# Kernel optimization log

Measured on AMD Instinct MI355X. Metric: run time of the kernel, lower is better.

Reference implementation:

```python
import jax, jax.numpy as jnp
import numpy as np

NEG = jnp.float32(-1e30)  # finite stand-in for -inf (keeps grads NaN-free)

B, S = 8, 256


def _inside_logZ(scores, mask):
    """CYK inside algorithm. scores/mask: [B, S, S]. Returns scalar logZ.

    Recurrence (widths w = 1..S-1, processed as a scan over anti-diagonals):
      s[i, i+1] = scores[i, i+1]
      s[i, i+w] = scores[i, i+w] + logsumexp_{k=i+1..i+w-1} (s[i, k] + s[k, i+w])
    logZ = sum_b s[b, 0, lens[b]].
    """
    Bsz, Sl, _ = scores.shape
    lens = mask[:, 0].sum(-1)                    # [B] sentence lengths
    idx = jnp.arange(Sl)
    rows = idx[:, None]                          # [S,1] span start i
    m = idx[None, :]                             # [1,S] split offset (k = i+m)
    km = jnp.clip(rows + m, 0, Sl - 1)           # [S,S] split index k, clipped reads

    def step(s, w):
        # s: [B,S,S] chart. Process all spans of width w at once.
        j = jnp.clip(rows + w, 0, Sl - 1)        # [S,1] span end (clipped)
        left = s[:, rows, km]                    # s[b, i, i+m]      -> [B,S,S]
        right = s[:, km, j]                      # s[b, i+m, i+w]    -> [B,S,S]
        valid = (m >= 1) & (m <= w - 1) & (rows + w < Sl)
        lse = jax.nn.logsumexp(jnp.where(valid, left + right, NEG), axis=-1)  # [B,S]
        diag = scores[:, idx, jnp.clip(idx + w, 0, Sl - 1)]                    # [B,S]
        val = diag + jnp.where(w == 1, 0.0, lse)
        # scatter onto the w-th diagonal; out-of-range (i+w >= S) lanes dropped
        s = s.at[:, idx, idx + w].set(val, mode='drop')
        return s, None

    s0 = jnp.full((Bsz, Sl, Sl), NEG, scores.dtype)
    s, _ = jax.lax.scan(step, s0, jnp.arange(1, Sl))
    return s[jnp.arange(Bsz), 0, lens].sum()


def setup_inputs() -> dict:
    key = jax.random.key(0)
    scores = jax.random.normal(key, (B, S, S), dtype=jnp.float32)
    # strict upper-triangular mask (all sentences full length S-1 tokens)
    mask = jnp.triu(jnp.ones((S, S), dtype=bool), k=1)
    mask = jnp.broadcast_to(mask, (B, S, S))
    return {"scores": scores, "mask": mask}


def reference(scores, mask):
    # forward(scores, mask, target=None, mbr=True): marginals = d logZ / d scores
    marginals = jax.grad(lambda sc: _inside_logZ(sc, mask))(scores)
    return marginals
```

## Files before the change

kernel.cpp:

```cpp
#include <hip/hip_runtime.h>

#define SL 256
#define BATCH 8
#define NT 1024
#define W0 16
#define LDSF 33152
#define TABN 264
#define LDSB ((LDSF + 32 + TABN + 3 * 256) * 4)

__device__ __forceinline__ int rowOff(int j) {
  int jp = (j > 128) ? (256 - j) : j;
  int base = (jp - 1) * 260;
  if (j > 128) base += (jp + 3) & ~3;
  return base;
}

template <int G>
__device__ __forceinline__ float grpSum(float v) {
#pragma unroll
  for (int o = G >> 1; o; o >>= 1) v += __shfl_xor(v, o, 64);
  return v;
}

__device__ __forceinline__ void barrier_lgkm() {
  __builtin_amdgcn_sched_barrier(0);
  asm volatile("s_waitcnt lgkmcnt(0)" ::: "memory");
  __builtin_amdgcn_s_barrier();
  __builtin_amdgcn_sched_barrier(0);
}

__device__ void rescaleE(int tid, float dc, int wcur, float* sh,
                         float* Es1, float* Es2, float* Es3,
                         const int* __restrict__ tab) {
  const int lane = tid & 63, wave = tid >> 6;
  for (int j = 1 + wave; j < SL; j += 16) {
    int jlo = j - wcur; if (jlo < 0) jlo = 0;
    int base = tab[j];
    for (int i = jlo + lane; i < j; i += 64)
      sh[base + i] *= __expf(-dc * (float)(j - i));
  }
  const float f1 = __expf(-dc);
  const float f2 = f1 * f1;
  const float f3 = f2 * f1;
  for (int x = tid; x < SL; x += NT) {
    Es1[x] *= f1; Es2[x] *= f2; Es3[x] *= f3;
  }
}

template <int G>
__device__ void insideP(int wlo, int whi, int t0, int tid,
                        const float* __restrict__ sc, float* __restrict__ sh,
                        float* __restrict__ red, const int* __restrict__ tab,
                        float* __restrict__ Es1, float* __restrict__ Es2,
                        float* __restrict__ Es3) {
  constexpr int LG = (G == 4) ? 2 : (G == 8) ? 3 : (G == 16) ? 4 : 5;
  constexpr int NG = 64 / G;
  const int lane = tid & 63, wv = tid >> 6;
  const int l = lane >> LG, lig = lane & (G - 1);
  const int i = wv * (NG - 1) + l;
  for (int w = wlo; w <= whi; w += 2) {
    const int t = t0 + ((w - wlo) >> 1);
    const float fl = red[16 + ((t - 1) & 1)];
    const unsigned wm1 = (unsigned)(w - 1);
    const unsigned wm2 = (unsigned)(w - 2);
    const bool vw = i < SL - w;
    const bool vw1 = (l < NG - 1) && (i < SL - w - 1);
    const int jw = (i + w < SL) ? i + w : SL - 1;
    const int jw1 = (i + w + 1 < SL) ? i + w + 1 : SL - 1;
    const int ojw = tab[jw], ojw1 = tab[jw1];
    const float scw = sc[i * SL + jw];
    const float scw1 = sc[i * SL + jw1];
    float a0 = 0.f, a1 = 0.f, b0 = 0.f, b1 = 0.f;
    if (vw) {
      for (int s4 = ((i + 1) & ~3) + 4 * lig; s4 < i + w; s4 += 4 * G) {
        float4 rw = *(const float4*)(sh + ojw + s4);
        float4 rw1 = *(const float4*)(sh + ojw1 + s4);
        int4 tv = *(const int4*)(tab + s4);
        float e0 = sh[tv.x + i], e1 = sh[tv.y + i];
        float e2 = sh[tv.z + i], e3 = sh[tv.w + i];
        const int d0 = s4 - i;
        float f0 = ((unsigned)(d0 - 1) < wm1) ? e0 : 0.f;
        float f1 = ((unsigned)(d0    ) < wm1) ? e1 : 0.f;
        float f2 = ((unsigned)(d0 + 1) < wm1) ? e2 : 0.f;
        float f3 = ((unsigned)(d0 + 2) < wm1) ? e3 : 0.f;
        a0 = fmaf(f0, rw.x, a0); a1 = fmaf(f1, rw.y, a1);
        a0 = fmaf(f2, rw.z, a0); a1 = fmaf(f3, rw.w, a1);
        float g0 = ((unsigned)(d0 - 2) < wm2) ? e0 : 0.f;
        float g1 = ((unsigned)(d0 - 1) < wm2) ? e1 : 0.f;
        float g2 = ((unsigned)(d0    ) < wm2) ? e2 : 0.f;
        float g3 = ((unsigned)(d0 + 1) < wm2) ? e3 : 0.f;
        b0 = fmaf(g0, rw1.x, b0); b1 = fmaf(g1, rw1.y, b1);
        b0 = fmaf(g2, rw1.z, b0); b1 = fmaf(g3, rw1.w, b1);
      }
    }
    float accw = grpSum<G>(a0 + a1);
    float accw1 = grpSum<G>(b0 + b1);
    float Ew = __expf(scw) * accw;
    if (vw && lig == 0) {
      sh[ojw + i] = Ew;
      if (accw > 3.5e19f || accw < 3e-16f) red[16 + (t & 1)] = fmaxf(accw, 1e-30f);
    }
    float EwN = __shfl_down(Ew, G, 64);
    if (vw1) {
      float tot = accw1 + Es1[i] * EwN + Ew * Es1[jw];
      if (lig == 0) {
        sh[ojw1 + i] = __expf(scw1) * tot;
        if (tot > 3.5e19f || tot < 3e-16f) red[16 + (t & 1)] = fmaxf(tot, 1e-30f);
      }
    }
    __syncthreads();
    if (fl != 0.f) {
      float dc = (__logf(fl) + 8.0f) / (float)(w - 2);
      rescaleE(tid, dc, w + 1, sh, Es1, Es2, Es3, tab);
      __syncthreads();
      if (tid == 0) { red[16] = 0.f; red[17] = 0.f; }
      __syncthreads();
    }
  }
}

template <int G>
__device__ void insideQ(int wlo, int whi, int t0, int tid,
                        const float* __restrict__ sc, float* __restrict__ sh,
                        float* __restrict__ red, const int* __restrict__ tab,
                        float* __restrict__ Es1, float* __restrict__ Es2,
                        float* __restrict__ Es3) {
  constexpr int LG = (G == 4) ? 2 : 3;
  constexpr int NG = 64 / G;
  constexpr int STR = 4 * G;
  const int lane = tid & 63, wv = tid >> 6;
  const int l = lane >> LG, lig = lane & (G - 1);
  const int i = wv * (NG - 3) + l;
  for (int w = wlo; w <= whi; w += 4) {
    const int t = t0 + ((w - wlo) >> 2);
    const float fl = red[16 + ((t - 1) & 1)];
    const bool v0 = i < SL - w;
    const bool v1 = i < SL - w - 1;
    const bool v2 = i < SL - w - 2;
    const bool v3 = i < SL - w - 3;
    const int j0 = (i + w < SL) ? i + w : SL - 1;
    const int j1 = (i + w + 1 < SL) ? i + w + 1 : SL - 1;
    const int j2 = (i + w + 2 < SL) ? i + w + 2 : SL - 1;
    const int j3 = (i + w + 3 < SL) ? i + w + 3 : SL - 1;
    const int o0 = tab[j0], o1 = tab[j1], o2 = tab[j2], o3 = tab[j3];
    const int rb = i * SL;
    const float s0 = sc[rb + j0], s1 = sc[rb + j1];
    const float s2 = sc[rb + j2], s3 = sc[rb + j3];
    float a0=0.f,a1=0.f,b0=0.f,b1=0.f,c0=0.f,c1=0.f,e4a=0.f,e4b=0.f;
    if (v0) {
      const int kend = i + w;
      const unsigned mA = (unsigned)(w - 1);
      const unsigned mB = (unsigned)(w - 2);
      const unsigned mC = (unsigned)(w - 3);
      const unsigned mD = (unsigned)(w - 4);
      auto mchunk = [&](int s4) {
        float4 r0 = *(const float4*)(sh + o0 + s4);
        float4 r1 = *(const float4*)(sh + o1 + s4);
        float4 r2 = *(const float4*)(sh + o2 + s4);
        float4 r3 = *(const float4*)(sh + o3 + s4);
        int4 tv = *(const int4*)(tab + s4);
        float e0 = sh[tv.x + i], e1 = sh[tv.y + i];
        float e2 = sh[tv.z + i], e3 = sh[tv.w + i];
        const int dd = s4 - i;
        float f0 = ((unsigned)(dd - 1) < mA) ? e0 : 0.f;
        float f1 = ((unsigned)(dd    ) < mA) ? e1 : 0.f;
        float f2 = ((unsigned)(dd + 1) < mA) ? e2 : 0.f;
        float f3 = ((unsigned)(dd + 2) < mA) ? e3 : 0.f;
        a0 = fmaf(f0, r0.x, a0); a1 = fmaf(f1, r0.y, a1);
        a0 = fmaf(f2, r0.z, a0); a1 = fmaf(f3, r0.w, a1);
        float g0 = ((unsigned)(dd - 2) < mB) ? e0 : 0.f;
        float g1 = ((unsigned)(dd - 1) < mB) ? e1 : 0.f;
        float g2 = ((unsigned)(dd    ) < mB) ? e2 : 0.f;
        float g3 = ((unsigned)(dd + 1) < mB) ? e3 : 0.f;
        b0 = fmaf(g0, r1.x, b0); b1 = fmaf(g1, r1.y, b1);
        b0 = fmaf(g2, r1.z, b0); b1 = fmaf(g3, r1.w, b1);
        float h0 = ((unsigned)(dd - 3) < mC) ? e0 : 0.f;
        float h1 = ((unsigned)(dd - 2) < mC) ? e1 : 0.f;
        float h2 = ((unsigned)(dd - 1) < mC) ? e2 : 0.f;
        float h3 = ((unsigned)(dd    ) < mC) ? e3 : 0.f;
        c0 = fmaf(h0, r2.x, c0); c1 = fmaf(h1, r2.y, c1);
        c0 = fmaf(h2, r2.z, c0); c1 = fmaf(h3, r2.w, c1);
        float k0 = ((unsigned)(dd - 4) < mD) ? e0 : 0.f;
        float k1 = ((unsigned)(dd - 3) < mD) ? e1 : 0.f;
        float k2 = ((unsigned)(dd - 2) < mD) ? e2 : 0.f;
        float k3 = ((unsigned)(dd - 1) < mD) ? e3 : 0.f;
        e4a = fmaf(k0, r3.x, e4a); e4b = fmaf(k1, r3.y, e4b);
        e4a = fmaf(k2, r3.z, e4a); e4b = fmaf(k3, r3.w, e4b);
      };
      int s4 = ((i + 1) & ~3) + 4 * lig;
      if (s4 < kend) { mchunk(s4); s4 += STR; }
      for (; s4 + 4 <= kend; s4 += STR) {
        float4 r0 = *(const float4*)(sh + o0 + s4);
        float4 r1 = *(const float4*)(sh + o1 + s4);
        float4 r2 = *(const float4*)(sh + o2 + s4);
        float4 r3 = *(const float4*)(sh + o3 + s4);
        int4 tv = *(const int4*)(tab + s4);
        float e0 = sh[tv.x + i], e1 = sh[tv.y + i];
        float e2 = sh[tv.z + i], e3 = sh[tv.w + i];
        a0 = fmaf(e0, r0.x, a0); a1 = fmaf(e1, r0.y, a1);
        a0 = fmaf(e2, r0.z, a0); a1 = fmaf(e3, r0.w, a1);
        b0 = fmaf(e0, r1.x, b0); b1 = fmaf(e1, r1.y, b1);
        b0 = fmaf(e2, r1.z, b0); b1 = fmaf(e3, r1.w, b1);
        c0 = fmaf(e0, r2.x, c0); c1 = fmaf(e1, r2.y, c1);
        c0 = fmaf(e2, r2.z, c0); c1 = fmaf(e3, r2.w, c1);
        e4a = fmaf(e0, r3.x, e4a); e4b = fmaf(e1, r3.y, e4b);
        e4a = fmaf(e2, r3.z, e4a); e4b = fmaf(e3, r3.w, e4b);
      }
      for (; s4 < kend; s4 += STR) mchunk(s4);
    }
    float A0 = grpSum<G>(a0 + a1);
    float A1 = grpSum<G>(b0 + b1);
    float A2 = grpSum<G>(c0 + c1);
    float A3 = grpSum<G>(e4a + e4b);
    const float es1i = Es1[i], es2i = Es2[i], es3i = Es3[i];
    const float E0 = __expf(s0) * A0;
    const float n10 = __shfl_down(E0, G, 64);
    const float n20 = __shfl_down(E0, 2 * G, 64);
    const float n30 = __shfl_down(E0, 3 * G, 64);
    const float T1 = A1 + es1i * n10 + E0 * Es1[j0];
    const float E1v = __expf(s1) * T1;
    const float n11 = __shfl_down(E1v, G, 64);
    const float n21 = __shfl_down(E1v, 2 * G, 64);
    const float T2 = A2 + es1i * n11 + E1v * Es1[j1] + es2i * n20 + E0 * Es2[j0];
    const float E2v = __expf(s2) * T2;
    const float n12 = __shfl_down(E2v, G, 64);
    const float T3 = A3 + es1i * n12 + E2v * Es1[j2] + es2i * n21 + E1v * Es2[j1]
                        + es3i * n30 + E0 * Es3[j0];
    const float E3v = __expf(s3) * T3;
    if (lig == 0) {
      if (v0)                sh[o0 + i] = E0;
      if (v1 && l <= NG - 2) sh[o1 + i] = E1v;
      if (v2 && l <= NG - 3) sh[o2 + i] = E2v;
      if (v3 && l <= NG - 4) sh[o3 + i] = E3v;
      if (v0 && (A0 > 3.5e19f || A0 < 3e-16f)) red[16 + (t & 1)] = fmaxf(A0, 1e-30f);
      if (v3 && l <= NG - 4 && (T3 > 3.5e19f || T3 < 3e-16f))
        red[16 + (t & 1)] = fmaxf(T3, 1e-30f);
    }
    __syncthreads();
    if (fl != 0.f) {
      float dc = (__logf(fl) + 8.0f) / (float)(w - 3);
      rescaleE(tid, dc, w + 3, sh, Es1, Es2, Es3, tab);
      __syncthreads();
      if (tid == 0) { red[16] = 0.f; red[17] = 0.f; }
      __syncthreads();
    }
  }
}

template <int G>
__device__ void outsideP(int wAhi, int wAlo, int tid, const float* __restrict__ sc,
                         float* __restrict__ gOut, const float* __restrict__ Eg,
                         const float* __restrict__ ETg, float* __restrict__ shH,
                         const int* __restrict__ tab, const float* __restrict__ Es1) {
  constexpr int LG = (G == 4) ? 2 : (G == 8) ? 3 : (G == 16) ? 4 : 5;
  constexpr int NG = 64 / G;
  const int lane = tid & 63, wv = tid >> 6;
  const int l = lane >> LG, lig = lane & (G - 1);
  const int p = wv * (NG - 1) + l;
  for (int wA = wAhi; wA >= wAlo; wA -= 2) {
    const int wB = wA - 1;
    const bool vA = p < SL - wA;
    const bool vB = (l >= 1 || wv == 0) && (p < SL - wB);
    const int qA = p + wA, qB = p + wB;
    const int qAc = (qA < SL) ? qA : SL - 1;
    const int qBc = (qB < SL) ? qB : SL - 1;
    const int oA = tab[qAc], oB = tab[qBc];
    const float scA = sc[p * SL + qAc];
    const float scB = sc[p * SL + qBc];
    float EpA = 0.f, EpB = 0.f;
    if (lig == 0) {
      if (vA) EpA = Eg[p * SL + qA];
      if (vB) EpB = Eg[p * SL + qB];
    }
    float a0 = 0.f, a1 = 0.f, b0 = 0.f, b1 = 0.f;
    if (vA || vB) {
      const float* erA = Eg + (size_t)qAc * SL;
      const float* erB = Eg + (size_t)qBc * SL;
      for (int s4 = ((qA + 1) & ~3) + 4 * lig; s4 < SL; s4 += 4 * G) {
        float4 eA = *(const float4*)(erA + s4);
        float4 eB = *(const float4*)(erB + s4);
        int4 tv = *(const int4*)(tab + s4);
        float h0 = shH[tv.x + p], h1 = shH[tv.y + p];
        float h2 = shH[tv.z + p], h3 = shH[tv.w + p];
        float m0 = (s4 + 0 > qA) ? h0 : 0.f, m1 = (s4 + 1 > qA) ? h1 : 0.f;
        float m2 = (s4 + 2 > qA) ? h2 : 0.f, m3 = (s4 + 3 > qA) ? h3 : 0.f;
        a0 = fmaf(eA.x, m0, a0); a1 = fmaf(eA.y, m1, a1);
        a0 = fmaf(eA.z, m2, a0); a1 = fmaf(eA.w, m3, a1);
        b0 = fmaf(eB.x, m0, b0); b1 = fmaf(eB.y, m1, b1);
        b0 = fmaf(eB.z, m2, b0); b1 = fmaf(eB.w, m3, b1);
      }
      for (int s4 = 4 * lig; s4 < p; s4 += 4 * G) {
        float4 ev = *(const float4*)(ETg + (size_t)p * SL + s4);
        float4 hA = *(const float4*)(shH + oA + s4);
        float4 hB = *(const float4*)(shH + oB + s4);
        a0 = fmaf(ev.x, hA.x, a0); a1 = fmaf(ev.y, hA.y, a1);
        a0 = fmaf(ev.z, hA.z, a0); a1 = fmaf(ev.w, hA.w, a1);
        float n0 = (s4 + 0 < p - 1) ? hB.x : 0.f;
        float n1 = (s4 + 1 < p - 1) ? hB.y : 0.f;
        float n2 = (s4 + 2 < p - 1) ? hB.z : 0.f;
        float n3 = (s4 + 3 < p - 1) ? hB.w : 0.f;
        b0 = fmaf(ev.x, n0, b0); b1 = fmaf(ev.y, n1, b1);
        b0 = fmaf(ev.z, n2, b0); b1 = fmaf(ev.w, n3, b1);
      }
    }
    float accA = grpSum<G>(a0 + a1);
    float accBb = grpSum<G>(b0 + b1);
    float HA = __expf(scA) * accA;
    if (vA && lig == 0) {
      shH[oA + p] = HA;
      gOut[p * SL + qA] = EpA * accA;
    }
    float HAup = __shfl_up(HA, G, 64);
    if (vB) {
      float accB = accBb + (vA ? Es1[qBc] * HA : 0.f)
                         + ((p > 0) ? Es1[p - 1] * HAup : 0.f);
      if (lig == 0) {
        shH[oB + p] = __expf(scB) * accB;
        gOut[p * SL + qB] = EpB * accB;
      }
    }
    barrier_lgkm();
  }
}

template <int G>
__device__ void outsideQ(int wAhi, int wAlo, int tid, const float* __restrict__ sc,
                         float* __restrict__ gOut, const float* __restrict__ Eg,
                         const float* __restrict__ ETg, float* __restrict__ shH,
                         const int* __restrict__ tab, const float* __restrict__ Es1,
                         const float* __restrict__ Es2, const float* __restrict__ Es3) {
  constexpr int LG = (G == 4) ? 2 : 3;
  constexpr int NG = 64 / G;
  constexpr int STR = 4 * G;
  const int lane = tid & 63, wv = tid >> 6;
  const int l = lane >> LG, lig = lane & (G - 1);
  const int p = wv * (NG - 3) + l;
  for (int wA = wAhi; wA >= wAlo; wA -= 4) {
    const bool v0 = p < SL - wA;
    const bool v1 = p < SL - wA + 1;
    const bool v2 = p < SL - wA + 2;
    const bool v3 = p < SL - wA + 3;
    const int q0 = p + wA, q1 = q0 - 1, q2 = q0 - 2, q3 = q0 - 3;
    const int qc0 = (q0 < SL) ? q0 : SL - 1;
    const int qc1 = (q1 < SL) ? q1 : SL - 1;
    const int qc2 = (q2 < SL) ? q2 : SL - 1;
    const int qc3 = (q3 < SL) ? q3 : SL - 1;
    const int o0 = tab[qc0], o1 = tab[qc1], o2 = tab[qc2], o3 = tab[qc3];
    const int rb = p * SL;
    const float s0 = sc[rb + qc0], s1 = sc[rb + qc1];
    const float s2 = sc[rb + qc2], s3 = sc[rb + qc3];
    float Ep0 = 0.f, Ep1 = 0.f, Ep2 = 0.f, Ep3 = 0.f;
    if (lig == 0) {
      if (v0) Ep0 = Eg[rb + q0];
      if (v1) Ep1 = Eg[rb + q1];
      if (v2) Ep2 = Eg[rb + q2];
      if (v3) Ep3 = Eg[rb + q3];
    }
    float a0=0.f,a1=0.f,b0=0.f,b1=0.f,c0=0.f,c1=0.f,e4a=0.f,e4b=0.f;
    if (v3) {
      const float* er0 = Eg + (size_t)qc0 * SL;
      const float* er1 = Eg + (size_t)qc1 * SL;
      const float* er2 = Eg + (size_t)qc2 * SL;
      const float* er3 = Eg + (size_t)qc3 * SL;
      int s4 = ((q0 + 1) & ~3) + 4 * lig;
      if (s4 < SL) {
        float4 e0v = *(const float4*)(er0 + s4);
        float4 e1v = *(const float4*)(er1 + s4);
        float4 e2v = *(const float4*)(er2 + s4);
        float4 e3v = *(const float4*)(er3 + s4);
        int4 tv = *(const int4*)(tab + s4);
        float h0 = (s4 + 0 > q0) ? shH[tv.x + p] : 0.f;
        float h1 = (s4 + 1 > q0) ? shH[tv.y + p] : 0.f;
        float h2 = (s4 + 2 > q0) ? shH[tv.z + p] : 0.f;
        float h3 = (s4 + 3 > q0) ? shH[tv.w + p] : 0.f;
        a0 = fmaf(e0v.x, h0, a0); a1 = fmaf(e0v.y, h1, a1);
        a0 = fmaf(e0v.z, h2, a0); a1 = fmaf(e0v.w, h3, a1);
        b0 = fmaf(e1v.x, h0, b0); b1 = fmaf(e1v.y, h1, b1);
        b0 = fmaf(e1v.z, h2, b0); b1 = fmaf(e1v.w, h3, b1);
        c0 = fmaf(e2v.x, h0, c0); c1 = fmaf(e2v.y, h1, c1);
        c0 = fmaf(e2v.z, h2, c0); c1 = fmaf(e2v.w, h3, c1);
        e4a = fmaf(e3v.x, h0, e4a); e4b = fmaf(e3v.y, h1, e4b);
        e4a = fmaf(e3v.z, h2, e4a); e4b = fmaf(e3v.w, h3, e4b);
        s4 += STR;
      }
      for (; s4 < SL; s4 += STR) {
        float4 e0v = *(const float4*)(er0 + s4);
        float4 e1v = *(const float4*)(er1 + s4);
        float4 e2v = *(const float4*)(er2 + s4);
        float4 e3v = *(const float4*)(er3 + s4);
        int4 tv = *(const int4*)(tab + s4);
        float h0 = shH[tv.x + p], h1 = shH[tv.y + p];
        float h2 = shH[tv.z + p], h3 = shH[tv.w + p];
        a0 = fmaf(e0v.x, h0, a0); a1 = fmaf(e0v.y, h1, a1);
        a0 = fmaf(e0v.z, h2, a0); a1 = fmaf(e0v.w, h3, a1);
        b0 = fmaf(e1v.x, h0, b0); b1 = fmaf(e1v.y, h1, b1);
        b0 = fmaf(e1v.z, h2, b0); b1 = fmaf(e1v.w, h3, b1);
        c0 = fmaf(e2v.x, h0, c0); c1 = fmaf(e2v.y, h1, c1);
        c0 = fmaf(e2v.z, h2, c0); c1 = fmaf(e2v.w, h3, c1);
        e4a = fmaf(e3v.x, h0, e4a); e4b = fmaf(e3v.y, h1, e4b);
        e4a = fmaf(e3v.z, h2, e4a); e4b = fmaf(e3v.w, h3, e4b);
      }
      const float* etr = ETg + (size_t)p * SL;
      int s5 = 4 * lig;
      for (; s5 + 4 <= p - 3; s5 += STR) {
        float4 ev = *(const float4*)(etr + s5);
        float4 h0v = *(const float4*)(shH + o0 + s5);
        float4 h1v = *(const float4*)(shH + o1 + s5);
        float4 h2v = *(const float4*)(shH + o2 + s5);
        float4 h3v = *(const float4*)(shH + o3 + s5);
        a0 = fmaf(ev.x, h0v.x, a0); a1 = fmaf(ev.y, h0v.y, a1);
        a0 = fmaf(ev.z, h0v.z, a0); a1 = fmaf(ev.w, h0v.w, a1);
        b0 = fmaf(ev.x, h1v.x, b0); b1 = fmaf(ev.y, h1v.y, b1);
        b0 = fmaf(ev.z, h1v.z, b0); b1 = fmaf(ev.w, h1v.w, b1);
        c0 = fmaf(ev.x, h2v.x, c0); c1 = fmaf(ev.y, h2v.y, c1);
        c0 = fmaf(ev.z, h2v.z, c0); c1 = fmaf(ev.w, h2v.w, c1);
        e4a = fmaf(ev.x, h3v.x, e4a); e4b = fmaf(ev.y, h3v.y, e4b);
        e4a = fmaf(ev.z, h3v.z, e4a); e4b = fmaf(ev.w, h3v.w, e4b);
      }
      for (; s5 < p; s5 += STR) {
        float4 ev = *(const float4*)(etr + s5);
        float4 h0v = *(const float4*)(shH + o0 + s5);
        float4 h1v = *(const float4*)(shH + o1 + s5);
        float4 h2v = *(const float4*)(shH + o2 + s5);
        float4 h3v = *(const float4*)(shH + o3 + s5);
        a0 = fmaf(ev.x, h0v.x, a0); a1 = fmaf(ev.y, h0v.y, a1);
        a0 = fmaf(ev.z, h0v.z, a0); a1 = fmaf(ev.w, h0v.w, a1);
        float n0 = (s5 + 0 < p - 1) ? h1v.x : 0.f;
        float n1 = (s5 + 1 < p - 1) ? h1v.y : 0.f;
        float n2 = (s5 + 2 < p - 1) ? h1v.z : 0.f;
        float n3 = (s5 + 3 < p - 1) ? h1v.w : 0.f;
        b0 = fmaf(ev.x, n0, b0); b1 = fmaf(ev.y, n1, b1);
        b0 = fmaf(ev.z, n2, b0); b1 = fmaf(ev.w, n3, b1);
        float x0 = (s5 + 0 < p - 2) ? h2v.x : 0.f;
        float x1 = (s5 + 1 < p - 2) ? h2v.y : 0.f;
        float x2 = (s5 + 2 < p - 2) ? h2v.z : 0.f;
        float x3 = (s5 + 3 < p - 2) ? h2v.w : 0.f;
        c0 = fmaf(ev.x, x0, c0); c1 = fmaf(ev.y, x1, c1);
        c0 = fmaf(ev.z, x2, c0); c1 = fmaf(ev.w, x3, c1);
        float y0 = (s5 + 0 < p - 3) ? h3v.x : 0.f;
        float y1 = (s5 + 1 < p - 3) ? h3v.y : 0.f;
        float y2 = (s5 + 2 < p - 3) ? h3v.z : 0.f;
        float y3 = (s5 + 3 < p - 3) ? h3v.w : 0.f;
        e4a = fmaf(ev.x, y0, e4a); e4b = fmaf(ev.y, y1, e4b);
        e4a = fmaf(ev.z, y2, e4a); e4b = fmaf(ev.w, y3, e4b);
      }
    }
    float A0 = grpSum<G>(a0 + a1);
    float A1 = grpSum<G>(b0 + b1);
    float A2 = grpSum<G>(c0 + c1);
    float A3 = grpSum<G>(e4a + e4b);
    const float ep1 = (p >= 1) ? Es1[p - 1] : 0.f;
    const float ep2 = (p >= 2) ? Es2[p - 2] : 0.f;
    const float ep3 = (p >= 3) ? Es3[p - 3] : 0.f;
    const float H0 = __expf(s0) * A0;
    const float u10 = __shfl_up(H0, G, 64);
    const float u20 = __shfl_up(H0, 2 * G, 64);
    const float u30 = __shfl_up(H0, 3 * G, 64);
    const float T1 = A1 + (v0 ? Es1[qc1] * H0 : 0.f) + ep1 * u10;
    const float H1 = __expf(s1) * T1;
    const float u11 = __shfl_up(H1, G, 64);
    const float u21 = __shfl_up(H1, 2 * G, 64);
    const float T2 = A2 + (v1 ? Es1[qc2] * H1 : 0.f) + ep1 * u11
                        + (v0 ? Es2[qc2] * H0 : 0.f) + ep2 * u20;
    const float H2 = __expf(s2) * T2;
    const float u12 = __shfl_up(H2, G, 64);
    const float T3 = A3 + (v2 ? Es1[qc3] * H2 : 0.f) + ep1 * u12
                        + (v1 ? Es2[qc3] * H1 : 0.f) + ep2 * u21
                        + (v0 ? Es3[qc3] * H0 : 0.f) + ep3 * u30;
    const float H3 = __expf(s3) * T3;
    const bool okl1 = (l >= 1) || (wv == 0);
    const bool okl2 = (l >= 2) || (wv == 0);
    const bool okl3 = (l >= 3) || (wv == 0);
    if (lig == 0) {
      if (v0)         { shH[o0 + p] = H0; gOut[rb + q0] = Ep0 * A0; }
      if (v1 && okl1) { shH[o1 + p] = H1; gOut[rb + q1] = Ep1 * T1; }
      if (v2 && okl2) { shH[o2 + p] = H2; gOut[rb + q2] = Ep2 * T2; }
      if (v3 && okl3) { shH[o3 + p] = H3; gOut[rb + q3] = Ep3 * T3; }
    }
    barrier_lgkm();
  }
}

template <int G>
__device__ void outsideB(int w0, int w1, int tid,
    const float* __restrict__ sc, float* __restrict__ gOut,
    const float* __restrict__ Eg, const float* __restrict__ ETg,
    float* __restrict__ shH, const int* __restrict__ tab) {
  constexpr int LG = (G == 4) ? 2 : (G == 8) ? 3 : (G == 16) ? 4 : (G == 32) ? 5 : 6;
  const int c = tid >> LG, lig = tid & (G - 1);
  for (int w = w0; w >= w1; --w) {
    if (c < SL - w) {
      const int p = c, q = p + w;
      float scv = 0.f, Epq = 0.f;
      if (lig == 0) { scv = sc[p * SL + q]; Epq = Eg[p * SL + q]; }
      float a0 = 0.f, a1 = 0.f;
      const float* er = Eg + (size_t)q * SL;
      for (int s4 = ((q + 1) & ~3) + 4 * lig; s4 < SL; s4 += 4 * G) {
        float4 ev = *(const float4*)(er + s4);
        int4 tv = *(const int4*)(tab + s4);
        float h0 = shH[tv.x + p], h1 = shH[tv.y + p];
        float h2 = shH[tv.z + p], h3 = shH[tv.w + p];
        a0 = fmaf(ev.x, (s4 + 0 > q) ? h0 : 0.f, a0);
        a1 = fmaf(ev.y, (s4 + 1 > q) ? h1 : 0.f, a1);
        a0 = fmaf(ev.z, (s4 + 2 > q) ? h2 : 0.f, a0);
        a1 = fmaf(ev.w, (s4 + 3 > q) ? h3 : 0.f, a1);
      }
      if (p > 0) {
        const float* et = ETg + (size_t)p * SL;
        const float* hq = shH + tab[q];
        for (int s4 = 4 * lig; s4 < p; s4 += 4 * G) {
          float4 ev = *(const float4*)(et + s4);
          float4 hv = *(const float4*)(hq + s4);
          a0 = fmaf(ev.x, hv.x, a0);
          a1 = fmaf(ev.y, hv.y, a1);
          a0 = fmaf(ev.z, hv.z, a0);
          a1 = fmaf(ev.w, hv.w, a1);
        }
      }
      float acc = grpSum<G>(a0 + a1);
      if (lig == 0) {
        gOut[p * SL + q] = Epq * acc;
        shH[tab[q] + p] = acc * __expf(scv);
      }
    }
    barrier_lgkm();
  }
}

__global__ __launch_bounds__(NT) void cyk_quad(
    const float* __restrict__ scores, float* __restrict__ out,
    float* __restrict__ ws) {
  extern __shared__ float sh[];
  float* red = sh + LDSF;
  int* tab = (int*)(sh + LDSF + 32);
  float* Es1 = sh + LDSF + 32 + TABN;
  float* Es2 = Es1 + 256;
  float* Es3 = Es2 + 256;
  const int b = blockIdx.x;
  const int tid = threadIdx.x;
  const int lane = tid & 63;
  const int wave = tid >> 6;
  const size_t P = (size_t)SL * SL;
  const float* sc = scores + (size_t)b * P;
  float* g   = out + (size_t)b * P;
  float* Eg  = ws + (size_t)b * P;
  float* ETg = ws + (size_t)(BATCH + b) * P;

  for (int idx = tid * 4; idx < LDSF; idx += NT * 4)
    *(float4*)(sh + idx) = make_float4(0.f, 0.f, 0.f, 0.f);
  if (tid < 32) red[tid] = 0.f;
  if (tid < TABN) tab[tid] = (tid >= 1 && tid <= 255) ? rowOff(tid) : 0;
  if (tid < 256) { Es1[tid] = 0.f; Es2[tid] = 0.f; Es3[tid] = 0.f; }
  __syncthreads();

  for (int i = tid; i < SL - 1; i += NT)
    sh[tab[i + 1] + i] = sc[i * SL + i + 1];
  __syncthreads();

  {
    const int c4 = tid >> 2, lig = tid & 3;
    for (int w = 2; w <= W0; ++w) {
      if (c4 < SL - w) {
        const int i = c4, j = i + w;
        const int oj = tab[j];
        float scv = 0.f;
        if (lig == 0) scv = sc[i * SL + j];
        float m = -1e30f, sum = 0.f;
        for (int k = i + 1 + lig; k < j; k += 4) {
          float t = sh[tab[k] + i] + sh[oj + k];
          float nm = fmaxf(m, t);
          sum = sum * __expf(m - nm) + __expf(t - nm);
          m = nm;
        }
#pragma unroll
        for (int o = 2; o; o >>= 1) {
          float mo = __shfl_xor(m, o, 64);
          float so = __shfl_xor(sum, o, 64);
          float nm = fmaxf(m, mo);
          sum = sum * __expf(m - nm) + so * __expf(mo - nm);
          m = nm;
        }
        if (lig == 0) sh[oj + i] = scv + m + __logf(sum);
      }
      __syncthreads();
    }
  }

  {
    int idx = tid < SL - W0 ? tid : SL - W0 - 1;
    float v = sh[tab[idx + W0] + idx];
#pragma unroll
    for (int o = 32; o; o >>= 1) v = fmaxf(v, __shfl_xor(v, o, 64));
    if (lane == 0) red[wave] = v;
  }
  __syncthreads();
  float cc;
  {
    float mx = red[0];
#pragma unroll
    for (int t = 1; t < 16; ++t) mx = fmaxf(mx, red[t]);
    cc = mx / (float)W0;
  }

  for (int w = 1; w <= W0; ++w) {
    for (int i = tid; i < SL - w; i += NT) {
      int o = tab[i + w] + i;
      float E = __expf(sh[o] - cc * (float)w);
      sh[o] = E;
      if (w == 1) Es1[i] = E;
      if (w == 2) Es2[i] = E;
      if (w == 3) Es3[i] = E;
    }
  }
  if (tid == 0) { red[16] = 0.f; red[17] = 0.f; }
  __syncthreads();

  insideP<4>(17, 43, 1, tid, sc, sh, red, tab, Es1, Es2, Es3);
  insideQ<4>(45, 169, 15, tid, sc, sh, red, tab, Es1, Es2, Es3);
  insideQ<8>(173, 249, 47, tid, sc, sh, red, tab, Es1, Es2, Es3);
  insideP<32>(253, 253, 67, tid, sc, sh, red, tab, Es1, Es2, Es3);

  {
    float acc = 0.f;
    if (wave == 0) {
      const int o255 = tab[255];
      for (int k = 1 + lane; k < 255; k += 64)
        acc += sh[tab[k]] * sh[o255 + k];
#pragma unroll
      for (int o = 32; o; o >>= 1) acc += __shfl_xor(acc, o, 64);
      if (lane == 0) sh[o255] = __expf(sc[SL - 1]) * acc;
    }
    __syncthreads();
  }

  for (int idx = tid; idx < SL * SL; idx += NT) {
    int j = idx >> 8, i = idx & 255;
    if (i < j) ETg[idx] = sh[tab[j] + i];
  }
  for (int idx = tid; idx < SL * SL; idx += NT) {
    int i = idx >> 8, k = idx & 255;
    if (k > i) Eg[idx] = sh[tab[k] + i];
  }
  if (tid == 0) {
    float Er = sh[tab[SL - 1]];
    red[20] = (Er > 0.f) ? __expf(sc[SL - 1]) / Er : 0.f;
    g[SL - 1] = 1.0f;
  }
  __syncthreads();

  for (int idx = tid * 4; idx < LDSF; idx += NT * 4)
    *(float4*)(sh + idx) = make_float4(0.f, 0.f, 0.f, 0.f);
  __syncthreads();
  if (tid == 0) sh[tab[SL - 1]] = red[20];
  __syncthreads();

  outsideP<32>(254, 254, tid, sc, g, Eg, ETg, sh, tab, Es1);
  outsideQ<8>(252, 176, tid, sc, g, Eg, ETg, sh, tab, Es1, Es2, Es3);
  outsideQ<4>(172, 48, tid, sc, g, Eg, ETg, sh, tab, Es1, Es2, Es3);
  outsideP<4>(44, 18, tid, sc, g, Eg, ETg, sh, tab, Es1);
  outsideB<4>(16, 1, tid, sc, g, Eg, ETg, sh, tab);
}

__device__ __forceinline__ float grpMaxR(float v, int G) {
#pragma unroll
  for (int o = 32; o; o >>= 1)
    if (o < G) v = fmaxf(v, __shfl_xor(v, o, 64));
  return v;
}
__device__ __forceinline__ float grpSumR(float v, int G) {
#pragma unroll
  for (int o = 32; o; o >>= 1)
    if (o < G) v += __shfl_xor(v, o, 64);
  return v;
}

__global__ __launch_bounds__(NT) void cyk_io_fb(
    const float* __restrict__ scores, float* __restrict__ out,
    float* __restrict__ ws) {
  const int b = blockIdx.x;
  const int tid = threadIdx.x;
  const size_t P = (size_t)SL * SL;
  const float* sc = scores + (size_t)b * P;
  float* g = out + (size_t)b * P;
  float* s = ws + (size_t)b * P;
  float* l = ws + (size_t)(BATCH + b) * P;

  for (int i = tid; i < SL - 1; i += NT) {
    s[i * SL + i + 1] = sc[i * SL + i + 1];
    l[i * SL + i + 1] = 0.f;
  }
  __syncthreads();

  for (int w = 2; w < SL; ++w) {
    const int cells = SL - w;
    int G = NT / cells;
    G = (G >= 64) ? 64 : (1 << (31 - __clz(G)));
    const int lg = 31 - __clz(G);
    const int c = tid >> lg;
    const int lig = tid & (G - 1);
    if (c < cells) {
      const int i = c, j = i + w;
      const float* srow = s + i * SL;
      float m = -INFINITY;
      for (int k = i + 1 + lig; k < j; k += G)
        m = fmaxf(m, srow[k] + s[k * SL + j]);
      m = grpMaxR(m, G);
      float sum = 0.f;
      for (int k = i + 1 + lig; k < j; k += G)
        sum += __expf(srow[k] + s[k * SL + j] - m);
      sum = grpSumR(sum, G);
      if (lig == 0) {
        const float lse = m + __logf(sum);
        s[i * SL + j] = sc[i * SL + j] + lse;
        l[i * SL + j] = lse;
      }
    }
    __syncthreads();
  }

  if (tid == 0) g[0 * SL + (SL - 1)] = 1.0f;
  __syncthreads();

  for (int w = SL - 2; w >= 1; --w) {
    const int cells = SL - w;
    int G = NT / cells;
    G = (G >= 64) ? 64 : (1 << (31 - __clz(G)));
    const int lg = 31 - __clz(G);
    const int c = tid >> lg;
    const int lig = tid & (G - 1);
    if (c < cells) {
      const int p = c, q = p + w;
      const float spq = s[p * SL + q];
      const int TR = SL - 1 - q;
      const int T = TR + p;
      float acc = 0.f;
      for (int t = lig; t < T; t += G) {
        if (t < TR) {
          const int j = q + 1 + t;
          acc += g[p * SL + j] * __expf(spq + s[q * SL + j] - l[p * SL + j]);
        } else {
          const int i = t - TR;
          acc += g[i * SL + q] * __expf(s[i * SL + p] + spq - l[i * SL + q]);
        }
      }
      acc = grpSumR(acc, G);
      if (lig == 0) g[p * SL + q] = acc;
    }
    __syncthreads();
  }
}

extern "C" void kernel_launch(void* const* d_in, const int* in_sizes, int n_in,
                              void* d_out, int out_size, void* d_ws, size_t ws_size,
                              hipStream_t stream) {
  const float* scores = (const float*)d_in[0];
  float* out = (float*)d_out;
  float* ws = (float*)d_ws;

  const size_t sq = (size_t)SL * SL * sizeof(float);
  hipMemsetAsync(d_out, 0, (size_t)BATCH * sq, stream);

  int dev = 0;
  hipGetDevice(&dev);
  int maxShm = 0;
  hipDeviceGetAttribute(&maxShm, hipDeviceAttributeMaxSharedMemoryPerBlock, dev);
  (void)hipFuncSetAttribute(reinterpret_cast<const void*>(cyk_quad),
                            hipFuncAttributeMaxDynamicSharedMemorySize, LDSB);

  if (maxShm >= LDSB && ws_size >= (size_t)2 * BATCH * sq) {
    hipMemsetAsync(ws, 0, (size_t)2 * BATCH * sq, stream);
    cyk_quad<<<BATCH, NT, LDSB, stream>>>(scores, out, ws);
  } else {
    cyk_io_fb<<<BATCH, NT, 0, stream>>>(scores, out, ws);
  }
}
```

Measured before the change: 651.2 us.

## Process eight anti-diagonals per barrier in inside and outside passes

Adds insideO/outsideO variants that compute eight consecutive CYK widths per iteration and close the intra-block dependencies with shuffles and the first seven diagonal-energy tables. The mid-range widths are reassigned to these variants, which cuts the number of block-wide barriers and lets the shared left/right operand loads be reused across eight outputs. In exchange each thread needs more registers, does redundant triangular-correction work, uses fewer useful rows per wave (NG-7), and the LDS footprint grows by four extra Es rows.

After: 726.4 us. 1.12x slower.

```diff
diff --git a/kernel.cpp b/kernel.cpp
--- a/kernel.cpp
+++ b/kernel.cpp
@@ -6,7 +6,7 @@
 #define W0 16
 #define LDSF 33152
 #define TABN 264
-#define LDSB ((LDSF + 32 + TABN + 3 * 256) * 4)
+#define LDSB ((LDSF + 32 + TABN + 7 * 256) * 4)
 
 __device__ __forceinline__ int rowOff(int j) {
   int jp = (j > 128) ? (256 - j) : j;
@@ -29,8 +29,7 @@
   __builtin_amdgcn_sched_barrier(0);
 }
 
-__device__ void rescaleE(int tid, float dc, int wcur, float* sh,
-                         float* Es1, float* Es2, float* Es3,
+__device__ void rescaleE(int tid, float dc, int wcur, float* sh, float* Es,
                          const int* __restrict__ tab) {
   const int lane = tid & 63, wave = tid >> 6;
   for (int j = 1 + wave; j < SL; j += 16) {
@@ -40,10 +39,10 @@
       sh[base + i] *= __expf(-dc * (float)(j - i));
   }
   const float f1 = __expf(-dc);
-  const float f2 = f1 * f1;
-  const float f3 = f2 * f1;
   for (int x = tid; x < SL; x += NT) {
-    Es1[x] *= f1; Es2[x] *= f2; Es3[x] *= f3;
+    float fd = f1;
+#pragma unroll
+    for (int d = 0; d < 7; ++d) { Es[d * 256 + x] *= fd; fd *= f1; }
   }
 }
 
@@ -51,10 +50,10 @@
 __device__ void insideP(int wlo, int whi, int t0, int tid,
                         const float* __restrict__ sc, float* __restrict__ sh,
                         float* __restrict__ red, const int* __restrict__ tab,
-                        float* __restrict__ Es1, float* __restrict__ Es2,
-                        float* __restrict__ Es3) {
+                        float* __restrict__ Es) {
   constexpr int LG = (G == 4) ? 2 : (G == 8) ? 3 : (G == 16) ? 4 : 5;
   constexpr int NG = 64 / G;
+  const float* Es1 = Es;
   const int lane = tid & 63, wv = tid >> 6;
   const int l = lane >> LG, lig = lane & (G - 1);
   const int i = wv * (NG - 1) + l;
@@ -111,7 +110,7 @@
     __syncthreads();
     if (fl != 0.f) {
       float dc = (__logf(fl) + 8.0f) / (float)(w - 2);
-      rescaleE(tid, dc, w + 1, sh, Es1, Es2, Es3, tab);
+      rescaleE(tid, dc, w + 1, sh, Es, tab);
       __syncthreads();
       if (tid == 0) { red[16] = 0.f; red[17] = 0.f; }
       __syncthreads();
@@ -123,11 +122,13 @@
 __device__ void insideQ(int wlo, int whi, int t0, int tid,
                         const float* __restrict__ sc, float* __restrict__ sh,
                         float* __restrict__ red, const int* __restrict__ tab,
-                        float* __restrict__ Es1, float* __restrict__ Es2,
-                        float* __restrict__ Es3) {
+                        float* __restrict__ Es) {
   constexpr int LG = (G == 4) ? 2 : 3;
   constexpr int NG = 64 / G;
   constexpr int STR = 4 * G;
+  const float* Es1 = Es;
+  const float* Es2 = Es + 256;
+  const float* Es3 = Es + 512;
   const int lane = tid & 63, wv = tid >> 6;
   const int l = lane >> LG, lig = lane & (G - 1);
   const int i = wv * (NG - 3) + l;
@@ -239,7 +240,108 @@
     __syncthreads();
     if (fl != 0.f) {
       float dc = (__logf(fl) + 8.0f) / (float)(w - 3);
-      rescaleE(tid, dc, w + 3, sh, Es1, Es2, Es3, tab);
+      rescaleE(tid, dc, w + 3, sh, Es, tab);
+      __syncthreads();
+      if (tid == 0) { red[16] = 0.f; red[17] = 0.f; }
+      __syncthreads();
+    }
+  }
+}
+
+template <int G>
+__device__ void insideO(int wlo, int whi, int t0, int tid,
+                        const float* __restrict__ sc, float* __restrict__ sh,
+                        float* __restrict__ red, const int* __restrict__ tab,
+                        float* __restrict__ Es) {
+  constexpr int LG = 2;
+  constexpr int NG = 64 / G;
+  constexpr int STR = 4 * G;
+  const int lane = tid & 63, wv = tid >> 6;
+  const int l = lane >> LG, lig = lane & (G - 1);
+  const int i = wv * (NG - 7) + l;
+  for (int w = wlo; w <= whi; w += 8) {
+    const int t = t0 + ((w - wlo) >> 3);
+    const float fl = red[16 + ((t - 1) & 1)];
+    bool vv[8]; int jj[8], om[8]; float ss[8];
+#pragma unroll
+    for (int m = 0; m < 8; ++m) {
+      vv[m] = i < SL - w - m;
+      jj[m] = (i + w + m < SL) ? (i + w + m) : (SL - 1);
+      om[m] = tab[jj[m]];
+      ss[m] = sc[i * SL + jj[m]];
+    }
+    float A0[8], A1[8];
+#pragma unroll
+    for (int m = 0; m < 8; ++m) { A0[m] = 0.f; A1[m] = 0.f; }
+    if (vv[0]) {
+      const int kend = i + w;
+      auto mchunk = [&](int s4) {
+        int4 tv = *(const int4*)(tab + s4);
+        float e0 = sh[tv.x + i], e1 = sh[tv.y + i];
+        float e2 = sh[tv.z + i], e3 = sh[tv.w + i];
+        const int dd = s4 - i;
+#pragma unroll
+        for (int m = 0; m < 8; ++m) {
+          float4 r = *(const float4*)(sh + om[m] + s4);
+          const unsigned lim = (unsigned)(w - 1 - m);
+          float f0 = ((unsigned)(dd - 1 - m) < lim) ? e0 : 0.f;
+          float f1 = ((unsigned)(dd     - m) < lim) ? e1 : 0.f;
+          float f2 = ((unsigned)(dd + 1 - m) < lim) ? e2 : 0.f;
+          float f3 = ((unsigned)(dd + 2 - m) < lim) ? e3 : 0.f;
+          A0[m] = fmaf(f0, r.x, A0[m]); A1[m] = fmaf(f1, r.y, A1[m]);
+          A0[m] = fmaf(f2, r.z, A0[m]); A1[m] = fmaf(f3, r.w, A1[m]);
+        }
+      };
+      int s4 = ((i + 1) & ~3) + 4 * lig;
+      if (s4 < kend) { mchunk(s4); s4 += STR; }
+      for (; s4 + 4 <= kend; s4 += STR) {
+        int4 tv = *(const int4*)(tab + s4);
+        float e0 = sh[tv.x + i], e1 = sh[tv.y + i];
+        float e2 = sh[tv.z + i], e3 = sh[tv.w + i];
+#pragma unroll
+        for (int m = 0; m < 8; ++m) {
+          float4 r = *(const float4*)(sh + om[m] + s4);
+          A0[m] = fmaf(e0, r.x, A0[m]); A1[m] = fmaf(e1, r.y, A1[m]);
+          A0[m] = fmaf(e2, r.z, A0[m]); A1[m] = fmaf(e3, r.w, A1[m]);
+        }
+      }
+      for (; s4 < kend; s4 += STR) mchunk(s4);
+    }
+    float Aw[8];
+#pragma unroll
+    for (int m = 0; m < 8; ++m) Aw[m] = grpSum<G>(A0[m] + A1[m]);
+    float es[8]; es[0] = 0.f;
+#pragma unroll
+    for (int d = 1; d < 8; ++d) es[d] = Es[(d - 1) * 256 + i];
+    float E[8];
+    const float Tlo = Aw[0];
+    E[0] = __expf(ss[0]) * Tlo;
+    float Thi = 0.f;
+#pragma unroll
+    for (int m = 1; m < 8; ++m) {
+      float tv = Aw[m];
+#pragma unroll
+      for (int d = 1; d <= m; ++d) {
+        float n = __shfl_down(E[m - d], d * G, 64);
+        tv = fmaf(es[d], n, tv);
+        tv = fmaf(E[m - d], Es[(d - 1) * 256 + jj[m - d]], tv);
+      }
+      if (m == 7) Thi = tv;
+      E[m] = __expf(ss[m]) * tv;
+    }
+    if (lig == 0) {
+#pragma unroll
+      for (int m = 0; m < 8; ++m)
+        if (vv[m] && l <= NG - 1 - m) sh[om[m] + i] = E[m];
+      if (vv[0] && (Tlo > 3.5e19f || Tlo < 3e-16f))
+        red[16 + (t & 1)] = fmaxf(Tlo, 1e-30f);
+      if (vv[7] && l <= NG - 8 && (Thi > 3.5e19f || Thi < 3e-16f))
+        red[16 + (t & 1)] = fmaxf(Thi, 1e-30f);
+    }
+    __syncthreads();
+    if (fl != 0.f) {
+      float dc = (__logf(fl) + 8.0f) / (float)(w - 4);
+      rescaleE(tid, dc, w + 7, sh, Es, tab);
       __syncthreads();
       if (tid == 0) { red[16] = 0.f; red[17] = 0.f; }
       __syncthreads();
@@ -251,9 +353,10 @@
 __device__ void outsideP(int wAhi, int wAlo, int tid, const float* __restrict__ sc,
                          float* __restrict__ gOut, const float* __restrict__ Eg,
                          const float* __restrict__ ETg, float* __restrict__ shH,
-                         const int* __restrict__ tab, const float* __restrict__ Es1) {
+                         const int* __restrict__ tab, const float* __restrict__ Es) {
   constexpr int LG = (G == 4) ? 2 : (G == 8) ? 3 : (G == 16) ? 4 : 5;
   constexpr int NG = 64 / G;
+  const float* Es1 = Es;
   const int lane = tid & 63, wv = tid >> 6;
   const int l = lane >> LG, lig = lane & (G - 1);
   const int p = wv * (NG - 1) + l;
@@ -327,11 +430,13 @@
 __device__ void outsideQ(int wAhi, int wAlo, int tid, const float* __restrict__ sc,
                          float* __restrict__ gOut, const float* __restrict__ Eg,
                          const float* __restrict__ ETg, float* __restrict__ shH,
-                         const int* __restrict__ tab, const float* __restrict__ Es1,
-                         const float* __restrict__ Es2, const float* __restrict__ Es3) {
+                         const int* __restrict__ tab, const float* __restrict__ Es) {
   constexpr int LG = (G == 4) ? 2 : 3;
   constexpr int NG = 64 / G;
   constexpr int STR = 4 * G;
+  const float* Es1 = Es;
+  const float* Es2 = Es + 256;
+  const float* Es3 = Es + 512;
   const int lane = tid & 63, wv = tid >> 6;
   const int l = lane >> LG, lig = lane & (G - 1);
   const int p = wv * (NG - 3) + l;
@@ -482,6 +587,116 @@
 }
 
 template <int G>
+__device__ void outsideO(int wAhi, int wAlo, int tid, const float* __restrict__ sc,
+                         float* __restrict__ gOut, const float* __restrict__ Eg,
+                         const float* __restrict__ ETg, float* __restrict__ shH,
+                         const int* __restrict__ tab, const float* __restrict__ Es) {
+  constexpr int LG = 2;
+  constexpr int NG = 64 / G;
+  constexpr int STR = 4 * G;
+  const int lane = tid & 63, wv = tid >> 6;
+  const int l = lane >> LG, lig = lane & (G - 1);
+  const int p = wv * (NG - 7) + l;
+  const int rb = p * SL;
+  for (int wA = wAhi; wA >= wAlo; wA -= 8) {
+    bool vv[8]; int qc[8], oo[8]; float ss[8];
+#pragma unroll
+    for (int m = 0; m < 8; ++m) {
+      vv[m] = p < SL - wA + m;
+      int q = p + wA - m;
+      qc[m] = (q < SL) ? q : SL - 1;
+      oo[m] = tab[qc[m]];
+      ss[m] = sc[rb + qc[m]];
+    }
+    float A0[8], A1[8];
+#pragma unroll
+    for (int m = 0; m < 8; ++m) { A0[m] = 0.f; A1[m] = 0.f; }
+    if (vv[7]) {
+      const int q0 = p + wA;
+      int s4 = ((q0 + 1) & ~3) + 4 * lig;
+      if (s4 < SL) {
+        int4 tv = *(const int4*)(tab + s4);
+        float h0 = (s4 + 0 > q0) ? shH[tv.x + p] : 0.f;
+        float h1 = (s4 + 1 > q0) ? shH[tv.y + p] : 0.f;
+        float h2 = (s4 + 2 > q0) ? shH[tv.z + p] : 0.f;
+        float h3 = (s4 + 3 > q0) ? shH[tv.w + p] : 0.f;
+#pragma unroll
+        for (int m = 0; m < 8; ++m) {
+          float4 ev = *(const float4*)(Eg + (size_t)qc[m] * SL + s4);
+          A0[m] = fmaf(ev.x, h0, A0[m]); A1[m] = fmaf(ev.y, h1, A1[m]);
+          A0[m] = fmaf(ev.z, h2, A0[m]); A1[m] = fmaf(ev.w, h3, A1[m]);
+        }
+        s4 += STR;
+      }
+      for (; s4 < SL; s4 += STR) {
+        int4 tv = *(const int4*)(tab + s4);
+        float h0 = shH[tv.x + p], h1 = shH[tv.y + p];
+        float h2 = shH[tv.z + p], h3 = shH[tv.w + p];
+#pragma unroll
+        for (int m = 0; m < 8; ++m) {
+          float4 ev = *(const float4*)(Eg + (size_t)qc[m] * SL + s4);
+          A0[m] = fmaf(ev.x, h0, A0[m]); A1[m] = fmaf(ev.y, h1, A1[m]);
+          A0[m] = fmaf(ev.z, h2, A0[m]); A1[m] = fmaf(ev.w, h3, A1[m]);
+        }
+      }
+      const float* etr = ETg + (size_t)p * SL;
+      int s5 = 4 * lig;
+      for (; s5 + 4 <= p - 7; s5 += STR) {
+        float4 ev = *(const float4*)(etr + s5);
+#pragma unroll
+        for (int m = 0; m < 8; ++m) {
+          float4 hv = *(const float4*)(shH + oo[m] + s5);
+          A0[m] = fmaf(ev.x, hv.x, A0[m]); A1[m] = fmaf(ev.y, hv.y, A1[m]);
+          A0[m] = fmaf(ev.z, hv.z, A0[m]); A1[m] = fmaf(ev.w, hv.w, A1[m]);
+        }
+      }
+      for (; s5 < p; s5 += STR) {
+        float4 ev = *(const float4*)(etr + s5);
+#pragma unroll
+        for (int m = 0; m < 8; ++m) {
+          float4 hv = *(const float4*)(shH + oo[m] + s5);
+          float y0 = (s5 + 0 < p - m) ? hv.x : 0.f;
+          float y1 = (s5 + 1 < p - m) ? hv.y : 0.f;
+          float y2 = (s5 + 2 < p - m) ? hv.z : 0.f;
+          float y3 = (s5 + 3 < p - m) ? hv.w : 0.f;
+          A0[m] = fmaf(ev.x, y0, A0[m]); A1[m] = fmaf(ev.y, y1, A1[m]);
+          A0[m] = fmaf(ev.z, y2, A0[m]); A1[m] = fmaf(ev.w, y3, A1[m]);
+        }
+      }
+    }
+    float Aw[8];
+#pragma unroll
+    for (int m = 0; m < 8; ++m) Aw[m] = grpSum<G>(A0[m] + A1[m]);
+    float ep[8]; ep[0] = 0.f;
+#pragma unroll
+    for (int d = 1; d < 8; ++d) ep[d] = (p >= d) ? Es[(d - 1) * 256 + (p - d)] : 0.f;
+    float H[8];
+    H[0] = __expf(ss[0]) * Aw[0];
+#pragma unroll
+    for (int m = 1; m < 8; ++m) {
+      float tv = Aw[m];
+#pragma unroll
+      for (int d = 1; d <= m; ++d) {
+        float u = __shfl_up(H[m - d], d * G, 64);
+        tv = fmaf(ep[d], u, tv);
+        tv += (vv[m - d] ? Es[(d - 1) * 256 + qc[m]] : 0.f) * H[m - d];
+      }
+      H[m] = __expf(ss[m]) * tv;
+    }
+    if (lig == 0) {
+#pragma unroll
+      for (int m = 0; m < 8; ++m) {
+        if (vv[m] && (l >= m || wv == 0)) {
+          shH[oo[m] + p] = H[m];
+          gOut[rb + qc[m]] = Eg[rb + qc[m]] * H[m] * __expf(-ss[m]);
+        }
+      }
+    }
+    barrier_lgkm();
+  }
+}
+
+template <int G>
 __device__ void outsideB(int w0, int w1, int tid,
     const float* __restrict__ sc, float* __restrict__ gOut,
     const float* __restrict__ Eg, const float* __restrict__ ETg,
@@ -527,15 +742,13 @@
   }
 }
 
-__global__ __launch_bounds__(NT) void cyk_quad(
+__global__ __launch_bounds__(NT) void cyk_oct(
     const float* __restrict__ scores, float* __restrict__ out,
     float* __restrict__ ws) {
   extern __shared__ float sh[];
   float* red = sh + LDSF;
   int* tab = (int*)(sh + LDSF + 32);
-  float* Es1 = sh + LDSF + 32 + TABN;
-  float* Es2 = Es1 + 256;
-  float* Es3 = Es2 + 256;
+  float* Es = sh + LDSF + 32 + TABN;
   const int b = blockIdx.x;
   const int tid = threadIdx.x;
   const int lane = tid & 63;
@@ -550,7 +763,7 @@
     *(float4*)(sh + idx) = make_float4(0.f, 0.f, 0.f, 0.f);
   if (tid < 32) red[tid] = 0.f;
   if (tid < TABN) tab[tid] = (tid >= 1 && tid <= 255) ? rowOff(tid) : 0;
-  if (tid < 256) { Es1[tid] = 0.f; Es2[tid] = 0.f; Es3[tid] = 0.f; }
+  for (int x = tid; x < 7 * 256; x += NT) Es[x] = 0.f;
   __syncthreads();
 
   for (int i = tid; i < SL - 1; i += NT)
@@ -607,18 +820,17 @@
       int o = tab[i + w] + i;
       float E = __expf(sh[o] - cc * (float)w);
       sh[o] = E;
-      if (w == 1) Es1[i] = E;
-      if (w == 2) Es2[i] = E;
-      if (w == 3) Es3[i] = E;
+      if (w <= 7) Es[(w - 1) * 256 + i] = E;
     }
   }
   if (tid == 0) { red[16] = 0.f; red[17] = 0.f; }
   __syncthreads();
 
-  insideP<4>(17, 43, 1, tid, sc, sh, red, tab, Es1, Es2, Es3);
-  insideQ<4>(45, 169, 15, tid, sc, sh, red, tab, Es1, Es2, Es3);
-  insideQ<8>(173, 249, 47, tid, sc, sh, red, tab, Es1, Es2, Es3);
-  insideP<32>(253, 253, 67, tid, sc, sh, red, tab, Es1, Es2, Es3);
+  insideP<4>(17, 43, 1, tid, sc, sh, red, tab, Es);
+  insideQ<4>(45, 109, 15, tid, sc, sh, red, tab, Es);
+  insideO<4>(113, 241, 32, tid, sc, sh, red, tab, Es);
+  insideQ<8>(249, 249, 49, tid, sc, sh, red, tab, Es);
+  insideP<32>(253, 253, 50, tid, sc, sh, red, tab, Es);
 
   {
     float acc = 0.f;
@@ -654,11 +866,11 @@
   if (tid == 0) sh[tab[SL - 1]] = red[20];
   __syncthreads();
 
-  outsideP<32>(254, 254, tid, sc, g, Eg, ETg, sh, tab, Es1);
-  outsideQ<8>(252, 176, tid, sc, g, Eg, ETg, sh, tab, Es1, Es2, Es3);
-  outsideQ<4>(172, 48, tid, sc, g, Eg, ETg, sh, tab, Es1, Es2, Es3);
-  outsideP<4>(44, 18, tid, sc, g, Eg, ETg, sh, tab, Es1);
-  outsideB<4>(16, 1, tid, sc, g, Eg, ETg, sh, tab);
+  outsideP<32>(254, 254, tid, sc, g, Eg, ETg, sh, tab, Es);
+  outsideO<4>(252, 132, tid, sc, g, Eg, ETg, sh, tab, Es);
+  outsideQ<4>(124, 48, tid, sc, g, Eg, ETg, sh, tab, Es);
+  outsideP<4>(44, 16, tid, sc, g, Eg, ETg, sh, tab, Es);
+  outsideB<4>(14, 1, tid, sc, g, Eg, ETg, sh, tab);
 }
 
 __device__ __forceinline__ float grpMaxR(float v, int G) {
@@ -764,12 +976,12 @@
   hipGetDevice(&dev);
   int maxShm = 0;
   hipDeviceGetAttribute(&maxShm, hipDeviceAttributeMaxSharedMemoryPerBlock, dev);
-  (void)hipFuncSetAttribute(reinterpret_cast<const void*>(cyk_quad),
+  (void)hipFuncSetAttribute(reinterpret_cast<const void*>(cyk_oct),
                             hipFuncAttributeMaxDynamicSharedMemorySize, LDSB);
 
   if (maxShm >= LDSB && ws_size >= (size_t)2 * BATCH * sq) {
     hipMemsetAsync(ws, 0, (size_t)2 * BATCH * sq, stream);
-    cyk_quad<<<BATCH, NT, LDSB, stream>>>(scores, out, ws);
+    cyk_oct<<<BATCH, NT, LDSB, stream>>>(scores, out, ws);
   } else {
     cyk_io_fb<<<BATCH, NT, 0, stream>>>(scores, out, ws);
   }
```
